# Kernel optimization log

Hardware: AMD Instinct MI355X
Metric: run time of the kernel (lower is better)

Reference implementation:

```python
import jax, jax.numpy as jnp
import numpy as np

NEG_INF = float(-2**32 + 1)  # matches tf paddings = -2**32+1


def setup_inputs() -> dict:
    key = jax.random.key(0)
    k1, k2, k3 = jax.random.split(key, 3)
    B, T, U = 128, 8192, 64
    align = jax.random.normal(k1, (B, 1, T), dtype=jnp.float32)
    value = jax.random.normal(k2, (B, T, U), dtype=jnp.float32)
    key_masks = jax.random.randint(k3, (B, 1, T), 0, 2) > 0  # bool [B,1,T]
    return {"align": align, "value": value, "key_masks": key_masks}


def reference(align, value, key_masks):
    # mask-fill invalid positions with a very negative constant
    scores = jnp.where(key_masks, align, NEG_INF)           # [B,1,T]
    attn = jax.nn.softmax(scores, axis=-1)                  # [B,1,T]
    # dropout_rate=0 / inference: dropout is identity
    out = jnp.matmul(attn, value)                           # [B,1,U]
    return out
```

## Files before the change

### kernel.cpp

```cpp
#include <hip/hip_runtime.h>
#include <math.h>

#define NEG_INF_F (-4294967295.0f)

constexpr int B_ = 128;
constexpr int T_ = 8192;
constexpr int U_ = 64;
constexpr int NCHUNK = 8;
constexpr int CHUNK  = T_ / NCHUNK;

__global__ __launch_bounds__(1024) void k_weights(const float* __restrict__ align,
                                                  const int* __restrict__ mask,
                                                  float* __restrict__ w) {
  const int b   = blockIdx.x;
  const int tid = threadIdx.x;
  const size_t base = (size_t)b * T_;
  const float4* a4 = (const float4*)(align + base);
  const int4*   m4 = (const int4*)(mask + base);
  float4*       w4 = (float4*)(w + base);

  float4 av0 = a4[tid * 2 + 0];
  float4 av1 = a4[tid * 2 + 1];
  int4   mv0 = m4[tid * 2 + 0];
  int4   mv1 = m4[tid * 2 + 1];

  float sc[8];
  sc[0] = mv0.x ? av0.x : NEG_INF_F;
  sc[1] = mv0.y ? av0.y : NEG_INF_F;
  sc[2] = mv0.z ? av0.z : NEG_INF_F;
  sc[3] = mv0.w ? av0.w : NEG_INF_F;
  sc[4] = mv1.x ? av1.x : NEG_INF_F;
  sc[5] = mv1.y ? av1.y : NEG_INF_F;
  sc[6] = mv1.z ? av1.z : NEG_INF_F;
  sc[7] = mv1.w ? av1.w : NEG_INF_F;

  float lmax = sc[0];
#pragma unroll
  for (int i = 1; i < 8; i++) lmax = fmaxf(lmax, sc[i]);
#pragma unroll
  for (int off = 32; off > 0; off >>= 1) lmax = fmaxf(lmax, __shfl_xor(lmax, off));

  __shared__ float red[16];
  __shared__ float s_m, s_invl;
  const int wave = tid >> 6;
  if ((tid & 63) == 0) red[wave] = lmax;
  __syncthreads();
  if (tid < 16) {
    float v = red[tid];
#pragma unroll
    for (int off = 8; off > 0; off >>= 1) v = fmaxf(v, __shfl_xor(v, off));
    if (tid == 0) s_m = v;
  }
  __syncthreads();
  const float m = s_m;

  float e[8];
  float lsum = 0.f;
#pragma unroll
  for (int i = 0; i < 8; i++) { e[i] = __expf(sc[i] - m); lsum += e[i]; }
#pragma unroll
  for (int off = 32; off > 0; off >>= 1) lsum += __shfl_xor(lsum, off);
  if ((tid & 63) == 0) red[wave] = lsum;
  __syncthreads();
  if (tid < 16) {
    float v = red[tid];
#pragma unroll
    for (int off = 8; off > 0; off >>= 1) v += __shfl_xor(v, off);
    if (tid == 0) s_invl = 1.0f / v;
  }
  __syncthreads();
  const float invl = s_invl;

  w4[tid * 2 + 0] = make_float4(e[0] * invl, e[1] * invl, e[2] * invl, e[3] * invl);
  w4[tid * 2 + 1] = make_float4(e[4] * invl, e[5] * invl, e[6] * invl, e[7] * invl);
}

__global__ __launch_bounds__(256) void k_wsum(const float* __restrict__ value,
                                              const float* __restrict__ w,
                                              float* __restrict__ partial) {
  const int b     = blockIdx.x / NCHUNK;
  const int chunk = blockIdx.x % NCHUNK;
  const int tid   = threadIdx.x;
  const int grp   = tid >> 4;
  const int lane  = tid & 15;
  const float4* v4 = (const float4*)(value + (size_t)b * T_ * U_);
  const float*  wb = w + (size_t)b * T_;
  const int t0 = chunk * CHUNK;

  float4 acc = make_float4(0.f, 0.f, 0.f, 0.f);
#pragma unroll 4
  for (int it = 0; it < CHUNK / 16; ++it) {
    const int t = t0 + it * 16 + grp;
    const float wt = wb[t];
    const float4 v = v4[(size_t)t * 16 + lane];
    acc.x += wt * v.x;
    acc.y += wt * v.y;
    acc.z += wt * v.z;
    acc.w += wt * v.w;
  }

  __shared__ float4 lds[16][16];
  lds[grp][lane] = acc;
  __syncthreads();
#pragma unroll
  for (int s = 8; s > 0; s >>= 1) {
    if (grp < s) {
      float4 o = lds[grp + s][lane];
      acc.x += o.x; acc.y += o.y; acc.z += o.z; acc.w += o.w;
      lds[grp][lane] = acc;
    }
    __syncthreads();
  }
  if (grp == 0) {
    float4* p = (float4*)(partial + ((size_t)b * NCHUNK + chunk) * U_);
    p[lane] = acc;
  }
}

__global__ __launch_bounds__(256) void k_final(const float* __restrict__ partial,
                                               float* __restrict__ out) {
  const int idx = blockIdx.x * blockDim.x + threadIdx.x;
  const int b = idx / U_;
  const int u = idx % U_;
  const float* p = partial + (size_t)b * NCHUNK * U_ + u;
  float s = 0.f;
#pragma unroll
  for (int c = 0; c < NCHUNK; ++c) s += p[c * U_];
  out[idx] = s;
}

extern "C" void kernel_launch(void* const* d_in, const int* in_sizes, int n_in,
                              void* d_out, int out_size, void* d_ws, size_t ws_size,
                              hipStream_t stream) {
  const float* align = (const float*)d_in[0];
  const float* value = (const float*)d_in[1];
  const int*   mask  = (const int*)d_in[2];
  float* out = (float*)d_out;

  float* w       = (float*)d_ws;
  float* partial = w + (size_t)B_ * T_;

  k_weights<<<B_, 1024, 0, stream>>>(align, mask, w);
  k_wsum<<<B_ * NCHUNK, 256, 0, stream>>>(value, w, partial);
  k_final<<<(B_ * U_) / 256, 256, 0, stream>>>(partial, out);
}
```

Measured before the change: 52.41 us.

## Fuse softmax weight computation into weighted-sum kernel with redundant per-block softmax

Merges the softmax-weights kernel into the weighted-sum kernel: each of the 16 chunk blocks per batch row recomputes the full-row max and sum over all T elements, then keeps only its own chunk's normalized weights in shared memory. This drops one kernel launch and the global write and re-read of the weight buffer, and it doubles the chunk count to raise parallelism. Value loads now use nontemporal hints. The cost is 16x redundant reads of align and mask per row, plus a larger register footprint from holding 32 scores per thread.

After: 57.86 us. 10.4% more time.

```diff
diff --git a/kernel.cpp b/kernel.cpp
--- a/kernel.cpp
+++ b/kernel.cpp
@@ -3,116 +3,97 @@
 
 #define NEG_INF_F (-4294967295.0f)
 
+typedef float f4 __attribute__((ext_vector_type(4)));
+
 constexpr int B_ = 128;
 constexpr int T_ = 8192;
 constexpr int U_ = 64;
-constexpr int NCHUNK = 8;
+constexpr int NCHUNK = 16;
 constexpr int CHUNK  = T_ / NCHUNK;
 
-__global__ __launch_bounds__(1024) void k_weights(const float* __restrict__ align,
-                                                  const int* __restrict__ mask,
-                                                  float* __restrict__ w) {
-  const int b   = blockIdx.x;
-  const int tid = threadIdx.x;
-  const size_t base = (size_t)b * T_;
-  const float4* a4 = (const float4*)(align + base);
-  const int4*   m4 = (const int4*)(mask + base);
-  float4*       w4 = (float4*)(w + base);
+__global__ __launch_bounds__(256) void k_fused(const float* __restrict__ align,
+                                               const int* __restrict__ mask,
+                                               const float* __restrict__ value,
+                                               float* __restrict__ partial) {
+  const int b     = blockIdx.x / NCHUNK;
+  const int chunk = blockIdx.x % NCHUNK;
+  const int tid   = threadIdx.x;
 
-  float4 av0 = a4[tid * 2 + 0];
-  float4 av1 = a4[tid * 2 + 1];
-  int4   mv0 = m4[tid * 2 + 0];
-  int4   mv1 = m4[tid * 2 + 1];
+  const float4* a4 = (const float4*)(align + (size_t)b * T_);
+  const int4*   m4 = (const int4*)(mask + (size_t)b * T_);
 
-  float sc[8];
-  sc[0] = mv0.x ? av0.x : NEG_INF_F;
-  sc[1] = mv0.y ? av0.y : NEG_INF_F;
-  sc[2] = mv0.z ? av0.z : NEG_INF_F;
-  sc[3] = mv0.w ? av0.w : NEG_INF_F;
-  sc[4] = mv1.x ? av1.x : NEG_INF_F;
-  sc[5] = mv1.y ? av1.y : NEG_INF_F;
-  sc[6] = mv1.z ? av1.z : NEG_INF_F;
-  sc[7] = mv1.w ? av1.w : NEG_INF_F;
+  float sc[32];
+#pragma unroll
+  for (int j = 0; j < 8; ++j) {
+    const float4 av = a4[j * 256 + tid];
+    const int4   mv = m4[j * 256 + tid];
+    sc[j * 4 + 0] = mv.x ? av.x : NEG_INF_F;
+    sc[j * 4 + 1] = mv.y ? av.y : NEG_INF_F;
+    sc[j * 4 + 2] = mv.z ? av.z : NEG_INF_F;
+    sc[j * 4 + 3] = mv.w ? av.w : NEG_INF_F;
+  }
 
   float lmax = sc[0];
 #pragma unroll
-  for (int i = 1; i < 8; i++) lmax = fmaxf(lmax, sc[i]);
+  for (int i = 1; i < 32; ++i) lmax = fmaxf(lmax, sc[i]);
 #pragma unroll
   for (int off = 32; off > 0; off >>= 1) lmax = fmaxf(lmax, __shfl_xor(lmax, off));
 
-  __shared__ float red[16];
+  __shared__ float red[4];
   __shared__ float s_m, s_invl;
-  const int wave = tid >> 6;
-  if ((tid & 63) == 0) red[wave] = lmax;
+  if ((tid & 63) == 0) red[tid >> 6] = lmax;
   __syncthreads();
-  if (tid < 16) {
-    float v = red[tid];
-#pragma unroll
-    for (int off = 8; off > 0; off >>= 1) v = fmaxf(v, __shfl_xor(v, off));
-    if (tid == 0) s_m = v;
-  }
+  if (tid == 0) s_m = fmaxf(fmaxf(red[0], red[1]), fmaxf(red[2], red[3]));
   __syncthreads();
   const float m = s_m;
 
-  float e[8];
   float lsum = 0.f;
 #pragma unroll
-  for (int i = 0; i < 8; i++) { e[i] = __expf(sc[i] - m); lsum += e[i]; }
+  for (int i = 0; i < 32; ++i) { sc[i] = __expf(sc[i] - m); lsum += sc[i]; }
 #pragma unroll
   for (int off = 32; off > 0; off >>= 1) lsum += __shfl_xor(lsum, off);
-  if ((tid & 63) == 0) red[wave] = lsum;
+  if ((tid & 63) == 0) red[tid >> 6] = lsum;
   __syncthreads();
-  if (tid < 16) {
-    float v = red[tid];
-#pragma unroll
-    for (int off = 8; off > 0; off >>= 1) v += __shfl_xor(v, off);
-    if (tid == 0) s_invl = 1.0f / v;
-  }
+  if (tid == 0) s_invl = 1.0f / (red[0] + red[1] + red[2] + red[3]);
   __syncthreads();
   const float invl = s_invl;
 
-  w4[tid * 2 + 0] = make_float4(e[0] * invl, e[1] * invl, e[2] * invl, e[3] * invl);
-  w4[tid * 2 + 1] = make_float4(e[4] * invl, e[5] * invl, e[6] * invl, e[7] * invl);
-}
+  __shared__ float w_s[CHUNK];
+  if ((tid >> 7) == (chunk & 1)) {
+    const int jown = chunk >> 1;
+    const int k    = tid & 127;
+    ((float4*)w_s)[k] = make_float4(sc[jown * 4 + 0] * invl, sc[jown * 4 + 1] * invl,
+                                    sc[jown * 4 + 2] * invl, sc[jown * 4 + 3] * invl);
+  }
+  __syncthreads();
 
-__global__ __launch_bounds__(256) void k_wsum(const float* __restrict__ value,
-                                              const float* __restrict__ w,
-                                              float* __restrict__ partial) {
-  const int b     = blockIdx.x / NCHUNK;
-  const int chunk = blockIdx.x % NCHUNK;
-  const int tid   = threadIdx.x;
-  const int grp   = tid >> 4;
-  const int lane  = tid & 15;
-  const float4* v4 = (const float4*)(value + (size_t)b * T_ * U_);
-  const float*  wb = w + (size_t)b * T_;
-  const int t0 = chunk * CHUNK;
+  const int grp  = tid >> 4;
+  const int lane = tid & 15;
+  const f4* v4 = (const f4*)(value + (size_t)b * T_ * U_) +
+                 (size_t)chunk * CHUNK * 16;
 
-  float4 acc = make_float4(0.f, 0.f, 0.f, 0.f);
+  f4 acc = (f4)(0.f);
 #pragma unroll 4
   for (int it = 0; it < CHUNK / 16; ++it) {
-    const int t = t0 + it * 16 + grp;
-    const float wt = wb[t];
-    const float4 v = v4[(size_t)t * 16 + lane];
-    acc.x += wt * v.x;
-    acc.y += wt * v.y;
-    acc.z += wt * v.z;
-    acc.w += wt * v.w;
+    const int tl = it * 16 + grp;
+    const float wt = w_s[tl];
+    const f4 v = __builtin_nontemporal_load(&v4[(size_t)tl * 16 + lane]);
+    acc += wt * v;
   }
 
-  __shared__ float4 lds[16][16];
+  __shared__ f4 lds[16][16];
   lds[grp][lane] = acc;
   __syncthreads();
 #pragma unroll
   for (int s = 8; s > 0; s >>= 1) {
     if (grp < s) {
-      float4 o = lds[grp + s][lane];
-      acc.x += o.x; acc.y += o.y; acc.z += o.z; acc.w += o.w;
+      acc += lds[grp + s][lane];
       lds[grp][lane] = acc;
     }
     __syncthreads();
   }
   if (grp == 0) {
-    float4* p = (float4*)(partial + ((size_t)b * NCHUNK + chunk) * U_);
+    f4* p = (f4*)(partial + ((size_t)b * NCHUNK + chunk) * U_);
     p[lane] = acc;
   }
 }
@@ -137,10 +118,8 @@
   const int*   mask  = (const int*)d_in[2];
   float* out = (float*)d_out;
 
-  float* w       = (float*)d_ws;
-  float* partial = w + (size_t)B_ * T_;
+  float* partial = (float*)d_ws;
 
-  k_weights<<<B_, 1024, 0, stream>>>(align, mask, w);
-  k_wsum<<<B_ * NCHUNK, 256, 0, stream>>>(value, w, partial);
+  k_fused<<<B_ * NCHUNK, 256, 0, stream>>>(align, mask, value, partial);
   k_final<<<(B_ * U_) / 256, 256, 0, stream>>>(partial, out);
 }
```
